# Optimization experiments

Hardware: AMD Instinct MI355X
Metric: run time of the kernel (lower is better)

The kernel has to match this reference:

```python
import jax, jax.numpy as jnp
import numpy as np
from jax import lax

DIM = 384
NH = 8
HD = DIM // NH
M = 16          # num_anchors
B = 16
HH = 64
WW = 64
N = HH * WW
STD = 0.02


def setup_inputs() -> dict:
    key = jax.random.key(0)
    ks = jax.random.split(key, 12)
    rn = lambda k, shape: (jax.random.normal(k, shape, jnp.float32) * STD)
    return {
        "x": jax.random.normal(ks[0], (B, N, DIM), jnp.float32),
        "H": HH,
        "W": WW,
        "saliency_w": rn(ks[1], (DIM, 1)),
        "saliency_b": jnp.zeros((1,), jnp.float32),
        "anchor_seeds": rn(ks[2], (1, M, DIM)),
        "w_q_agg": rn(ks[3], (DIM, DIM)),
        "w_kv_agg": rn(ks[4], (DIM, 2 * DIM)),
        "w_q_self": rn(ks[5], (DIM, DIM)),
        "w_kv_self": rn(ks[6], (DIM, 2 * DIM)),
        "w_q_bcast": rn(ks[7], (DIM, DIM)),
        "w_kv_bcast": rn(ks[8], (DIM, 2 * DIM)),
        "dw_kernel": rn(ks[9], (DIM, 1, 3, 3)),  # depthwise conv, OIHW with I=1
        "w_proj": rn(ks[10], (DIM, DIM)),
    }


def _mhsa(q_in, kv_in, wq, wkv):
    """Multi-head cross attention. q_in: [B,Lq,C], kv_in: [B,Lk,C]."""
    b, lq, c = q_in.shape
    lk = kv_in.shape[1]
    scale = HD ** -0.5
    q = (q_in @ wq).reshape(b, lq, NH, HD)
    kv = (kv_in @ wkv).reshape(b, lk, 2, NH, HD)
    k, v = kv[:, :, 0], kv[:, :, 1]
    attn = jnp.einsum("bqhd,bkhd->bhqk", q, k) * scale
    attn = jax.nn.softmax(attn, axis=-1)
    out = jnp.einsum("bhqk,bkhd->bqhd", attn, v).reshape(b, lq, c)
    return out


def reference(x, H, W, saliency_w, saliency_b, anchor_seeds,
              w_q_agg, w_kv_agg, w_q_self, w_kv_self,
              w_q_bcast, w_kv_bcast, dw_kernel, w_proj):
    b, n, c = x.shape
    # saliency gating
    sal = jax.nn.sigmoid(x @ saliency_w + saliency_b)  # [B,N,1]
    x_sal = x * sal
    # stage 1: anchors aggregate from saliency-gated tokens
    anchors = jnp.broadcast_to(anchor_seeds, (b, M, c))
    anchors = anchors + _mhsa(anchors, x_sal, w_q_agg, w_kv_agg)
    # stage 2: anchor self-attention
    anchors = anchors + _mhsa(anchors, anchors, w_q_self, w_kv_self)
    # stage 3: broadcast anchors back to all tokens
    global_out = _mhsa(x, anchors, w_q_bcast, w_kv_bcast)
    # depthwise 3x3 conv on the 2D token map
    x2d = x.reshape(b, H, W, c).transpose(0, 3, 1, 2)  # NCHW
    local = lax.conv_general_dilated(
        x2d, dw_kernel, window_strides=(1, 1), padding="SAME",
        feature_group_count=c,
        dimension_numbers=("NCHW", "OIHW", "NCHW"))
    local = local.transpose(0, 2, 3, 1).reshape(b, n, c)
    return (global_out + local) @ w_proj
```

## Files before the change

kernel.cpp:

```cpp
#include <hip/hip_runtime.h>
#include <hip/hip_bf16.h>

#define SCALE 0.14433756729740643f

typedef __attribute__((ext_vector_type(8))) short bf16x8;
typedef __attribute__((ext_vector_type(4))) float f32x4;

template <typename T> __device__ inline T cvt_from_f(float v);
template <> __device__ inline float cvt_from_f<float>(float v) { return v; }
template <> __device__ inline __hip_bfloat16 cvt_from_f<__hip_bfloat16>(float v) { return __float2bfloat16(v); }

__device__ inline void gload16(const void* g, void* l) {
  __builtin_amdgcn_global_load_lds((const __attribute__((address_space(1))) void*)g,
                                   (__attribute__((address_space(3))) void*)l, 16, 0, 0);
}

__device__ inline int xcd_flat(int nwg) {
  int flat = (blockIdx.z * gridDim.y + blockIdx.y) * gridDim.x + blockIdx.x;
  int per = nwg >> 3;
  return (flat & 7) * per + (flat >> 3);
}

__global__ __launch_bounds__(256) void prep(const float* __restrict__ x,
                                            const float* __restrict__ wsal,
                                            const float* __restrict__ bsal,
                                            __hip_bfloat16* __restrict__ xb,
                                            float* __restrict__ sal) {
  int wave = threadIdx.x >> 6, lane = threadIdx.x & 63;
  size_t row = (size_t)blockIdx.x * 4 + wave;
  const float* xr = x + row * 384;
  float xs[6];
  float part = 0.f;
#pragma unroll
  for (int j = 0; j < 6; j++) {
    int c = lane + 64 * j;
    xs[j] = xr[c];
    part += xs[j] * wsal[c];
  }
#pragma unroll
  for (int off = 32; off >= 1; off >>= 1) part += __shfl_xor(part, off);
  float s = 1.f / (1.f + __expf(-(part + bsal[0])));
#pragma unroll
  for (int j = 0; j < 6; j++) {
    int c = lane + 64 * j;
    xb[row * 384 + c] = __float2bfloat16(xs[j]);
  }
  if (lane == 0) sal[row] = s;
}

__global__ void wcast_tv(const float* __restrict__ w, __hip_bfloat16* __restrict__ wt) {
  int idx = blockIdx.x * 256 + threadIdx.x;
  if (idx >= 384 * 384) return;
  int n = idx / 384, k = idx % 384;
  wt[idx] = __float2bfloat16(w[(size_t)k * 768 + 384 + n]);
}

template <int K, typename OT, int BSHIFT>
__global__ __launch_bounds__(256) void gemm_mfma(const __hip_bfloat16* __restrict__ A,
                                                 const __hip_bfloat16* __restrict__ BT,
                                                 OT* __restrict__ out, int Ncols,
                                                 size_t btBatchStride) {
  __shared__ __align__(16) __hip_bfloat16 Asl[128][32];
  __shared__ __align__(16) __hip_bfloat16 Bsl[128][32];
  int nf = xcd_flat(gridDim.x * gridDim.y);
  int bX = nf % gridDim.x, bY = nf / gridDim.x;
  int tid = threadIdx.x;
  int lane = tid & 63;
  int w = tid >> 6;
  int wr = w >> 1, wc = w & 1;
  int fr = lane & 15, fq = lane >> 4;
  int rowBase = bY * 128, colBase = bX * 128;
  const __hip_bfloat16* BTb = BT + (size_t)(rowBase >> BSHIFT) * btBatchStride;

  int r1 = tid >> 2, kc1 = tid & 3;
  int r2 = (tid + 256) >> 2;

  char* aB1 = (char*)Asl + (size_t)(w * 64) * 16;
  char* aB2 = (char*)Asl + (size_t)(256 + w * 64) * 16;
  char* bB1 = (char*)Bsl + (size_t)(w * 64) * 16;
  char* bB2 = (char*)Bsl + (size_t)(256 + w * 64) * 16;

  const __hip_bfloat16* a1 = A + (size_t)(rowBase + r1) * K + kc1 * 8;
  const __hip_bfloat16* a2 = A + (size_t)(rowBase + r2) * K + kc1 * 8;
  const __hip_bfloat16* b1 = BTb + (size_t)(colBase + r1) * K + kc1 * 8;
  const __hip_bfloat16* b2 = BTb + (size_t)(colBase + r2) * K + kc1 * 8;

  f32x4 acc[4][4] = {};

  for (int kk = 0; kk < K; kk += 32) {
    gload16(a1 + kk, aB1);
    gload16(a2 + kk, aB2);
    gload16(b1 + kk, bB1);
    gload16(b2 + kk, bB2);
    __syncthreads();
    bf16x8 af[4], bfv[4];
#pragma unroll
    for (int m = 0; m < 4; m++) af[m] = *(const bf16x8*)&Asl[wr * 64 + m * 16 + fr][fq * 8];
#pragma unroll
    for (int n = 0; n < 4; n++) bfv[n] = *(const bf16x8*)&Bsl[wc * 64 + n * 16 + fr][fq * 8];
#pragma unroll
    for (int m = 0; m < 4; m++)
#pragma unroll
      for (int n = 0; n < 4; n++)
        acc[m][n] = __builtin_amdgcn_mfma_f32_16x16x32_bf16(af[m], bfv[n], acc[m][n], 0, 0, 0);
    __syncthreads();
  }

#pragma unroll
  for (int m = 0; m < 4; m++) {
    int row0 = rowBase + wr * 64 + m * 16 + fq * 4;
#pragma unroll
    for (int n = 0; n < 4; n++) {
      int col = colBase + wc * 64 + n * 16 + fr;
      f32x4 v = acc[m][n];
#pragma unroll
      for (int r = 0; r < 4; r++) out[(size_t)(row0 + r) * Ncols + col] = cvt_from_f<OT>(v[r]);
    }
  }
}

__global__ __launch_bounds__(256) void gemm_vlog(const __hip_bfloat16* __restrict__ A,
                                                 const __hip_bfloat16* __restrict__ BT,
                                                 __hip_bfloat16* __restrict__ vT,
                                                 __hip_bfloat16* __restrict__ lgT,
                                                 const float* __restrict__ rowScale) {
  constexpr int K = 384;
  __shared__ __align__(16) __hip_bfloat16 Asl[128][32];
  __shared__ __align__(16) __hip_bfloat16 Bsl[128][32];
  int nf = xcd_flat(2048);
  int bX = nf & 3, bY = nf >> 2;
  int tid = threadIdx.x;
  int lane = tid & 63;
  int w = tid >> 6;
  int wr = w >> 1, wc = w & 1;
  int fr = lane & 15, fq = lane >> 4;
  int rowBase = bY * 128, colBase = bX * 128;

  int r1 = tid >> 2, kc1 = tid & 3;
  int r2 = (tid + 256) >> 2;

  char* aB1 = (char*)Asl + (size_t)(w * 64) * 16;
  char* aB2 = (char*)Asl + (size_t)(256 + w * 64) * 16;
  char* bB1 = (char*)Bsl + (size_t)(w * 64) * 16;
  char* bB2 = (char*)Bsl + (size_t)(256 + w * 64) * 16;

  const __hip_bfloat16* a1 = A + (size_t)(rowBase + r1) * K + kc1 * 8;
  const __hip_bfloat16* a2 = A + (size_t)(rowBase + r2) * K + kc1 * 8;
  const __hip_bfloat16* b1 = BT + (size_t)(colBase + r1) * K + kc1 * 8;
  const __hip_bfloat16* b2 = BT + (size_t)(colBase + r2) * K + kc1 * 8;

  f32x4 acc[4][4] = {};

  for (int kk = 0; kk < K; kk += 32) {
    gload16(a1 + kk, aB1);
    gload16(a2 + kk, aB2);
    gload16(b1 + kk, bB1);
    gload16(b2 + kk, bB2);
    __syncthreads();
    bf16x8 af[4], bfv[4];
#pragma unroll
    for (int m = 0; m < 4; m++) af[m] = *(const bf16x8*)&Asl[wr * 64 + m * 16 + fr][fq * 8];
#pragma unroll
    for (int n = 0; n < 4; n++) bfv[n] = *(const bf16x8*)&Bsl[wc * 64 + n * 16 + fr][fq * 8];
#pragma unroll
    for (int m = 0; m < 4; m++)
#pragma unroll
      for (int n = 0; n < 4; n++)
        acc[m][n] = __builtin_amdgcn_mfma_f32_16x16x32_bf16(af[m], bfv[n], acc[m][n], 0, 0, 0);
    __syncthreads();
  }

  float sv[4][4];
#pragma unroll
  for (int m = 0; m < 4; m++)
#pragma unroll
    for (int r = 0; r < 4; r++)
      sv[m][r] = rowScale[rowBase + wr * 64 + m * 16 + fq * 4 + r];

  if (bX < 3) {
#pragma unroll
    for (int m = 0; m < 4; m++) {
      int row0 = rowBase + wr * 64 + m * 16 + fq * 4;
      int bb = row0 >> 12;
      int n0 = row0 & 4095;
#pragma unroll
      for (int n = 0; n < 4; n++) {
        int col = colBase + wc * 64 + n * 16 + fr;
        __hip_bfloat16 tb[4];
#pragma unroll
        for (int r = 0; r < 4; r++) tb[r] = __float2bfloat16(acc[m][n][r] * sv[m][r]);
        *(unsigned long long*)(vT + ((size_t)bb * 384 + col) * 4096 + n0) = *(unsigned long long*)tb;
      }
    }
  } else {
#pragma unroll
    for (int m = 0; m < 4; m++) {
      int row0 = rowBase + wr * 64 + m * 16 + fq * 4;
      int bb = row0 >> 12;
      int n0 = row0 & 4095;
#pragma unroll
      for (int n = 0; n < 4; n++) {
        int col = wc * 64 + n * 16 + fr;
        __hip_bfloat16 tb[4];
#pragma unroll
        for (int r = 0; r < 4; r++) tb[r] = __float2bfloat16(acc[m][n][r] * sv[m][r]);
        *(unsigned long long*)(lgT + ((size_t)bb * 128 + col) * 4096 + n0) = *(unsigned long long*)tb;
      }
    }
  }
}

__global__ __launch_bounds__(256) void gemm_pv(const __hip_bfloat16* __restrict__ PT,
                                               const __hip_bfloat16* __restrict__ vT,
                                               float* __restrict__ pbuf) {
  __shared__ __align__(16) __hip_bfloat16 Asl[128][32];
  __shared__ __align__(16) __hip_bfloat16 Bsl[128][32];
  int nf = xcd_flat(384);
  int bX = nf % 3, bY = (nf / 3) & 15, kz = nf / 48;
  int tid = threadIdx.x;
  int lane = tid & 63;
  int w = tid >> 6;
  int wr = w >> 1, wc = w & 1;
  int fr = lane & 15, fq = lane >> 4;
  int rowBase = bY * 128, colBase = bX * 128;
  const __hip_bfloat16* BTb = vT + (size_t)bY * 384 * 4096;

  int r1 = tid >> 2, kc1 = tid & 3;
  int r2 = (tid + 256) >> 2;

  char* aB1 = (char*)Asl + (size_t)(w * 64) * 16;
  char* aB2 = (char*)Asl + (size_t)(256 + w * 64) * 16;
  char* bB1 = (char*)Bsl + (size_t)(w * 64) * 16;
  char* bB2 = (char*)Bsl + (size_t)(256 + w * 64) * 16;

  const __hip_bfloat16* a1 = PT + (size_t)(rowBase + r1) * 4096 + kz * 512 + kc1 * 8;
  const __hip_bfloat16* a2 = PT + (size_t)(rowBase + r2) * 4096 + kz * 512 + kc1 * 8;
  const __hip_bfloat16* b1 = BTb + (size_t)(colBase + r1) * 4096 + kz * 512 + kc1 * 8;
  const __hip_bfloat16* b2 = BTb + (size_t)(colBase + r2) * 4096 + kz * 512 + kc1 * 8;

  f32x4 acc[4][4] = {};

  for (int kk = 0; kk < 512; kk += 32) {
    gload16(a1 + kk, aB1);
    gload16(a2 + kk, aB2);
    gload16(b1 + kk, bB1);
    gload16(b2 + kk, bB2);
    __syncthreads();
    bf16x8 af[4], bfv[4];
#pragma unroll
    for (int m = 0; m < 4; m++) af[m] = *(const bf16x8*)&Asl[wr * 64 + m * 16 + fr][fq * 8];
#pragma unroll
    for (int n = 0; n < 4; n++) bfv[n] = *(const bf16x8*)&Bsl[wc * 64 + n * 16 + fr][fq * 8];
#pragma unroll
    for (int m = 0; m < 4; m++)
#pragma unroll
      for (int n = 0; n < 4; n++)
        acc[m][n] = __builtin_amdgcn_mfma_f32_16x16x32_bf16(af[m], bfv[n], acc[m][n], 0, 0, 0);
    __syncthreads();
  }

  float* outz = pbuf + (size_t)kz * 786432;
#pragma unroll
  for (int m = 0; m < 4; m++) {
    int row0 = rowBase + wr * 64 + m * 16 + fq * 4;
#pragma unroll
    for (int n = 0; n < 4; n++) {
      int col = colBase + wc * 64 + n * 16 + fr;
      f32x4 v = acc[m][n];
#pragma unroll
      for (int r = 0; r < 4; r++) outz[(size_t)(row0 + r) * 384 + col] = v[r];
    }
  }
}

__global__ void anch_fix2(const float* __restrict__ pbuf, const float* __restrict__ seeds,
                          float* __restrict__ anch1) {
  int idx = blockIdx.x * 256 + threadIdx.x;
  int b = idx / 6144;
  int rem = idx - b * 6144;
  int m = rem / 384, c = rem - m * 384;
  int g = b * 128 + (c / 48) * 16 + m;
  const float* p = pbuf + (size_t)g * 384 + c;
  float s = 0.f;
#pragma unroll
  for (int z = 0; z < 8; z++) s += p[(size_t)z * 786432];
  anch1[idx] = seeds[rem] + s;
}

__global__ __launch_bounds__(256) void softmax_rows(const __hip_bfloat16* __restrict__ lgT,
                                                    __hip_bfloat16* __restrict__ PT) {
  int g = blockIdx.x;
  const __hip_bfloat16* row = lgT + (size_t)g * 4096;
  int tid = threadIdx.x, wv = tid >> 6, lane = tid & 63;
  __shared__ float redm[4], reds[4];
  float v[16];
  union { ulonglong2 u; __hip_bfloat16 h[8]; } L0, L1;
  L0.u = *(const ulonglong2*)(row + tid * 16);
  L1.u = *(const ulonglong2*)(row + tid * 16 + 8);
#pragma unroll
  for (int i = 0; i < 8; i++) {
    v[i] = __bfloat162float(L0.h[i]);
    v[8 + i] = __bfloat162float(L1.h[i]);
  }
  float mx = v[0];
#pragma unroll
  for (int i = 1; i < 16; i++) mx = fmaxf(mx, v[i]);
#pragma unroll
  for (int off = 1; off < 64; off <<= 1) mx = fmaxf(mx, __shfl_xor(mx, off));
  if (lane == 0) redm[wv] = mx;
  __syncthreads();
  mx = fmaxf(fmaxf(redm[0], redm[1]), fmaxf(redm[2], redm[3]));
  float s = 0.f;
#pragma unroll
  for (int i = 0; i < 16; i++) {
    v[i] = __expf(v[i] - mx);
    s += v[i];
  }
#pragma unroll
  for (int off = 1; off < 64; off <<= 1) s += __shfl_xor(s, off);
  if (lane == 0) reds[wv] = s;
  __syncthreads();
  s = (reds[0] + reds[1]) + (reds[2] + reds[3]);
  float inv = 1.f / s;
  __hip_bfloat16 tb[16];
#pragma unroll
  for (int i = 0; i < 16; i++) tb[i] = __float2bfloat16(v[i] * inv);
  __hip_bfloat16* op = PT + (size_t)g * 4096 + tid * 16;
  *(ulonglong2*)op = *(ulonglong2*)tb;
  *(ulonglong2*)(op + 8) = *(ulonglong2*)(tb + 8);
}

__global__ void fill_wl(const float* __restrict__ wkv, const float* __restrict__ qseed,
                        __hip_bfloat16* __restrict__ wvlT) {
  int idx = blockIdx.x * 256 + threadIdx.x;
  int hm = idx / 384, ci = idx - hm * 384;
  int h = hm >> 4, m = hm & 15;
  const float* wp = wkv + (size_t)ci * 768 + h * 48;
  const float* qp = qseed + m * 384 + h * 48;
  float acc = 0.f;
#pragma unroll
  for (int d = 0; d < 48; d++) acc += wp[d] * qp[d];
  wvlT[384 * 384 + idx] = __float2bfloat16(acc);
}

__global__ __launch_bounds__(256) void wtrans(const float* __restrict__ wproj,
                                              __hip_bfloat16* __restrict__ bt2) {
  __shared__ float t[64][65];
  int kt = blockIdx.x * 64, ct = blockIdx.y * 64;
  int tid = threadIdx.x;
  int c = tid & 63, r4 = tid >> 6;
#pragma unroll
  for (int i = 0; i < 16; i++) {
    int r = i * 4 + r4;
    t[r][c] = wproj[(size_t)(kt + r) * 384 + ct + c];
  }
  __syncthreads();
  __hip_bfloat16 vals[16];
#pragma unroll
  for (int i = 0; i < 16; i++) vals[i] = __float2bfloat16(t[c][i * 4 + r4]);
  for (int b = blockIdx.z * 4; b < blockIdx.z * 4 + 4; b++) {
    __hip_bfloat16* dst = bt2 + (size_t)b * 196608;
#pragma unroll
    for (int i = 0; i < 16; i++) {
      int rr = i * 4 + r4;
      dst[(size_t)(ct + rr) * 512 + kt + c] = vals[i];
    }
  }
}

__global__ __launch_bounds__(256) void fill_fold(const float* __restrict__ wq,
                                                 const float* __restrict__ wproj,
                                                 const float* __restrict__ kvb,
                                                 __hip_bfloat16* __restrict__ wpbT,
                                                 __hip_bfloat16* __restrict__ bt2) {
  int b = blockIdx.y;
  int tid = threadIdx.x;
  __shared__ float stage[16][48];
  __shared__ __hip_bfloat16 obuf[16][264];
  if (blockIdx.x < 8) {
    int h = blockIdx.x;
    for (int idx = tid; idx < 768; idx += 256) {
      int m = idx / 48, d = idx % 48;
      stage[m][d] = kvb[(size_t)(b * 16 + m) * 768 + h * 48 + d];
    }
    __syncthreads();
    for (int kbase = 0; kbase < 384; kbase += 256) {
      int chunk = (kbase == 0) ? 256 : 128;
      if (tid < chunk) {
        int k = kbase + tid;
        const float4* wp = (const float4*)(wq + (size_t)k * 384 + h * 48);
        float acc[16] = {};
#pragma unroll
        for (int dq = 0; dq < 12; dq++) {
          float4 wv = wp[dq];
#pragma unroll
          for (int m = 0; m < 16; m++)
            acc[m] += stage[m][dq * 4] * wv.x + stage[m][dq * 4 + 1] * wv.y +
                      stage[m][dq * 4 + 2] * wv.z + stage[m][dq * 4 + 3] * wv.w;
        }
#pragma unroll
        for (int m = 0; m < 16; m++) obuf[m][tid] = __float2bfloat16(acc[m]);
      }
      __syncthreads();
      for (int widx = tid; widx < 16 * chunk; widx += 256) {
        int m = widx / chunk, kk = widx - m * chunk;
        wpbT[(size_t)b * 49152 + (size_t)(h * 16 + m) * 384 + kbase + kk] = obuf[m][kk];
      }
      __syncthreads();
    }
  } else {
    int h = blockIdx.x - 8;
    for (int idx = tid; idx < 768; idx += 256) {
      int m = idx / 48, d = idx % 48;
      stage[m][d] = kvb[(size_t)(b * 16 + m) * 768 + 384 + h * 48 + d];
    }
    __syncthreads();
    for (int cp = tid; cp < 384; cp += 256) {
      float acc[16] = {};
      for (int d = 0; d < 48; d++) {
        float wv = wproj[(size_t)(h * 48 + d) * 384 + cp];
#pragma unroll
        for (int m = 0; m < 16; m++) acc[m] += stage[m][d] * wv;
      }
      __hip_bfloat16 tb[16];
#pragma unroll
      for (int m = 0; m < 16; m++) tb[m] = __float2bfloat16(acc[m]);
      __hip_bfloat16* dst = bt2 + (size_t)b * 196608 + (size_t)cp * 512 + 384 + h * 16;
      *(ulonglong2*)dst = *(ulonglong2*)tb;
      *(ulonglong2*)(dst + 8) = *(ulonglong2*)(tb + 8);
    }
  }
}

__global__ __launch_bounds__(256) void pgemm(const __hip_bfloat16* __restrict__ A,
                                             const __hip_bfloat16* __restrict__ wpbT,
                                             __hip_bfloat16* __restrict__ A2) {
  constexpr int K = 384;
  __shared__ __align__(16) __hip_bfloat16 Asl[128][32];
  __shared__ __align__(16) __hip_bfloat16 Bsl[128][32];
  int tid = threadIdx.x;
  int lane = tid & 63;
  int w = tid >> 6;
  int wr = w >> 1, wc = w & 1;
  int fr = lane & 15, fq = lane >> 4;
  int rowBase = blockIdx.y * 128;
  const __hip_bfloat16* BTb = wpbT + (size_t)(rowBase >> 12) * (128 * 384);

  int r1 = tid >> 2, kc1 = tid & 3;
  int r2 = (tid + 256) >> 2;

  char* aB1 = (char*)Asl + (size_t)(w * 64) * 16;
  char* aB2 = (char*)Asl + (size_t)(256 + w * 64) * 16;
  char* bB1 = (char*)Bsl + (size_t)(w * 64) * 16;
  char* bB2 = (char*)Bsl + (size_t)(256 + w * 64) * 16;

  const __hip_bfloat16* a1 = A + (size_t)(rowBase + r1) * K + kc1 * 8;
  const __hip_bfloat16* a2 = A + (size_t)(rowBase + r2) * K + kc1 * 8;
  const __hip_bfloat16* b1 = BTb + (size_t)r1 * K + kc1 * 8;
  const __hip_bfloat16* b2 = BTb + (size_t)r2 * K + kc1 * 8;

  f32x4 acc[4][4] = {};

  for (int kk = 0; kk < K; kk += 32) {
    gload16(a1 + kk, aB1);
    gload16(a2 + kk, aB2);
    gload16(b1 + kk, bB1);
    gload16(b2 + kk, bB2);
    __syncthreads();
    bf16x8 af[4], bfv[4];
#pragma unroll
    for (int m = 0; m < 4; m++) af[m] = *(const bf16x8*)&Asl[wr * 64 + m * 16 + fr][fq * 8];
#pragma unroll
    for (int n = 0; n < 4; n++) bfv[n] = *(const bf16x8*)&Bsl[wc * 64 + n * 16 + fr][fq * 8];
#pragma unroll
    for (int m = 0; m < 4; m++)
#pragma unroll
      for (int n = 0; n < 4; n++)
        acc[m][n] = __builtin_amdgcn_mfma_f32_16x16x32_bf16(af[m], bfv[n], acc[m][n], 0, 0, 0);
    __syncthreads();
  }

#pragma unroll
  for (int m = 0; m < 4; m++) {
    int row0 = rowBase + wr * 64 + m * 16 + fq * 4;
#pragma unroll
    for (int n = 0; n < 4; n++) {
      int col = wc * 64 + n * 16 + fr;
      f32x4 v = acc[m][n];
      f32x4 mx = v;
#pragma unroll
      for (int off = 1; off < 16; off <<= 1)
#pragma unroll
        for (int r = 0; r < 4; r++) mx[r] = fmaxf(mx[r], __shfl_xor(mx[r], off));
      f32x4 e;
#pragma unroll
      for (int r = 0; r < 4; r++) e[r] = __expf(v[r] - mx[r]);
      f32x4 s = e;
#pragma unroll
      for (int off = 1; off < 16; off <<= 1)
#pragma unroll
        for (int r = 0; r < 4; r++) s[r] += __shfl_xor(s[r], off);
#pragma unroll
      for (int r = 0; r < 4; r++)
        A2[(size_t)(row0 + r) * 512 + 384 + col] = __float2bfloat16(e[r] / s[r]);
    }
  }
}

__global__ __launch_bounds__(256) void dwconv3(const __hip_bfloat16* __restrict__ xb,
                                               const float* __restrict__ dwk,
                                               __hip_bfloat16* __restrict__ A2) {
  int b = blockIdx.y;
  int y = blockIdx.x;
  int w = threadIdx.x >> 6, lane = threadIdx.x & 63;
  int c0 = lane * 6;
  int x0 = w * 16;
  float kw[9][6];
#pragma unroll
  for (int ki = 0; ki < 9; ki++)
#pragma unroll
    for (int i = 0; i < 6; i++) kw[ki][i] = dwk[(c0 + i) * 9 + ki];

  const __hip_bfloat16* base = xb + ((size_t)(b * 4096 + y * 64)) * 384 + c0;
  bool yv[3];
#pragma unroll
  for (int t = 0; t < 3; t++) {
    int yy = y + t - 1;
    yv[t] = (yy >= 0 && yy < 64);
  }

  float colL[3][6], colC[3][6], colR[3][6];
  auto loadcol = [&](float (&dst)[3][6], int x) {
#pragma unroll
    for (int t = 0; t < 3; t++) {
      if (yv[t]) {
        const __hip_bfloat16* p = base + ((size_t)(t - 1) * 64 + x) * 384;
#pragma unroll
        for (int i = 0; i < 6; i++) dst[t][i] = __bfloat162float(p[i]);
      } else {
#pragma unroll
        for (int i = 0; i < 6; i++) dst[t][i] = 0.f;
      }
    }
  };

  if (x0 == 0) {
#pragma unroll
    for (int t = 0; t < 3; t++)
#pragma unroll
      for (int i = 0; i < 6; i++) colL[t][i] = 0.f;
  } else {
    loadcol(colL, x0 - 1);
  }
  loadcol(colC, x0);

  for (int step = 0; step < 16; step++) {
    int x = x0 + step;
    if (x + 1 < 64) {
      loadcol(colR, x + 1);
    } else {
#pragma unroll
      for (int t = 0; t < 3; t++)
#pragma unroll
        for (int i = 0; i < 6; i++) colR[t][i] = 0.f;
    }
    float acc[6];
#pragma unroll
    for (int i = 0; i < 6; i++) {
      float a = 0.f;
#pragma unroll
      for (int t = 0; t < 3; t++)
        a += colL[t][i] * kw[t * 3 + 0][i] + colC[t][i] * kw[t * 3 + 1][i] +
             colR[t][i] * kw[t * 3 + 2][i];
      acc[i] = a;
    }
    __hip_bfloat16 tb[6];
#pragma unroll
    for (int i = 0; i < 6; i++) tb[i] = __float2bfloat16(acc[i]);
    __hip_bfloat16* gp = A2 + ((size_t)(b * 4096 + y * 64 + x)) * 512 + c0;
    *(unsigned int*)(gp) = *(unsigned int*)(tb);
    *(unsigned int*)(gp + 2) = *(unsigned int*)(tb + 2);
    *(unsigned int*)(gp + 4) = *(unsigned int*)(tb + 4);
#pragma unroll
    for (int t = 0; t < 3; t++)
#pragma unroll
      for (int i = 0; i < 6; i++) {
        colL[t][i] = colC[t][i];
        colC[t][i] = colR[t][i];
      }
  }
}

__global__ __launch_bounds__(256) void anchor_proj2(const float* __restrict__ A,
                                                    const float* __restrict__ W,
                                                    float* __restrict__ out, int wstride,
                                                    int scaleCols) {
  int cs = blockIdx.x * 16;
  int b = blockIdx.y;
  __shared__ float a1[16][385];
  int tid = threadIdx.x;
  for (int idx = tid; idx < 6144; idx += 256) a1[idx / 384][idx % 384] = A[b * 6144 + idx];
  __syncthreads();
  int m = tid >> 4, cc = tid & 15;
  int col = cs + cc;
  const float* wp = W + col;
  float acc0 = 0.f, acc1 = 0.f, acc2 = 0.f, acc3 = 0.f;
#pragma unroll 4
  for (int k = 0; k < 384; k += 4) {
    acc0 += a1[m][k] * wp[(size_t)k * wstride];
    acc1 += a1[m][k + 1] * wp[(size_t)(k + 1) * wstride];
    acc2 += a1[m][k + 2] * wp[(size_t)(k + 2) * wstride];
    acc3 += a1[m][k + 3] * wp[(size_t)(k + 3) * wstride];
  }
  float acc = (acc0 + acc1) + (acc2 + acc3);
  if (col < scaleCols) acc *= SCALE;
  out[((size_t)b * 16 + m) * wstride + col] = acc;
}

__global__ __launch_bounds__(256) void anchor_proj_qkv(const float* __restrict__ A,
                                                       const float* __restrict__ Wq,
                                                       const float* __restrict__ Wkv,
                                                       float* __restrict__ q_out,
                                                       float* __restrict__ kv_out) {
  bool isQ = blockIdx.x < 24;
  int bx = isQ ? blockIdx.x : blockIdx.x - 24;
  const float* W = isQ ? Wq : Wkv;
  float* outp = isQ ? q_out : kv_out;
  int wstride = isQ ? 384 : 768;
  float scale = isQ ? SCALE : 1.f;
  int cs = bx * 16;
  int b = blockIdx.y;
  __shared__ float a1[16][385];
  int tid = threadIdx.x;
  for (int idx = tid; idx < 6144; idx += 256) a1[idx / 384][idx % 384] = A[b * 6144 + idx];
  __syncthreads();
  int m = tid >> 4, cc = tid & 15;
  int col = cs + cc;
  const float* wp = W + col;
  float acc0 = 0.f, acc1 = 0.f, acc2 = 0.f, acc3 = 0.f;
#pragma unroll 4
  for (int k = 0; k < 384; k += 4) {
    acc0 += a1[m][k] * wp[(size_t)k * wstride];
    acc1 += a1[m][k + 1] * wp[(size_t)(k + 1) * wstride];
    acc2 += a1[m][k + 2] * wp[(size_t)(k + 2) * wstride];
    acc3 += a1[m][k + 3] * wp[(size_t)(k + 3) * wstride];
  }
  float acc = ((acc0 + acc1) + (acc2 + acc3)) * scale;
  outp[((size_t)b * 16 + m) * wstride + col] = acc;
}

__global__ void self_attn(const float* __restrict__ qsf, const float* __restrict__ kvs,
                          const float* __restrict__ anch1, float* __restrict__ anch2) {
  int h = blockIdx.x & 7, b = blockIdx.x >> 3;
  __shared__ float qs[16][48], ks[16][48], vs[16][48], p[16][17];
  int tid = threadIdx.x;
  for (int idx = tid; idx < 768; idx += 256) {
    int m = idx / 48, d = idx % 48;
    qs[m][d] = qsf[(b * 16 + m) * 384 + h * 48 + d];
    ks[m][d] = kvs[(b * 16 + m) * 768 + h * 48 + d];
    vs[m][d] = kvs[(b * 16 + m) * 768 + 384 + h * 48 + d];
  }
  __syncthreads();
  {
    int mq = tid >> 4, mk = tid & 15;
    float acc = 0.f;
    for (int d = 0; d < 48; d++) acc += qs[mq][d] * ks[mk][d];
    p[mq][mk] = acc;
  }
  __syncthreads();
  if (tid < 16) {
    float mx = -1e30f;
    for (int mk = 0; mk < 16; mk++) mx = fmaxf(mx, p[tid][mk]);
    float sum = 0.f;
    for (int mk = 0; mk < 16; mk++) {
      float e = __expf(p[tid][mk] - mx);
      p[tid][mk] = e;
      sum += e;
    }
    float inv = 1.f / sum;
    for (int mk = 0; mk < 16; mk++) p[tid][mk] *= inv;
  }
  __syncthreads();
  for (int idx = tid; idx < 768; idx += 256) {
    int m = idx / 48, d = idx % 48;
    float acc = 0.f;
    for (int mk = 0; mk < 16; mk++) acc += p[m][mk] * vs[mk][d];
    int c = h * 48 + d;
    anch2[(b * 16 + m) * 384 + c] = anch1[(b * 16 + m) * 384 + c] + acc;
  }
}

extern "C" void kernel_launch(void* const* d_in, const int* in_sizes, int n_in,
                              void* d_out, int out_size, void* d_ws, size_t ws_size,
                              hipStream_t stream) {
  (void)in_sizes; (void)n_in; (void)out_size; (void)ws_size;
  const float* x = (const float*)d_in[0];
  const float* wsal = (const float*)d_in[3];
  const float* bsal = (const float*)d_in[4];
  const float* seeds = (const float*)d_in[5];
  const float* w_q_agg = (const float*)d_in[6];
  const float* w_kv_agg = (const float*)d_in[7];
  const float* w_q_self = (const float*)d_in[8];
  const float* w_kv_self = (const float*)d_in[9];
  const float* w_q_bcast = (const float*)d_in[10];
  const float* w_kv_bcast = (const float*)d_in[11];
  const float* dwk = (const float*)d_in[12];
  const float* w_proj = (const float*)d_in[13];
  float* out = (float*)d_out;

  char* ws = (char*)d_ws;
  size_t off = 0;
  auto take = [&](size_t bytes) -> void* {
    void* p = ws + off;
    off += (bytes + 255) & ~(size_t)255;
    return p;
  };
  __hip_bfloat16* xb = (__hip_bfloat16*)take(50331648);
  __hip_bfloat16* vT = (__hip_bfloat16*)take(50331648);
  char* lgRegion = (char*)take(33554432);
  __hip_bfloat16* PT = (__hip_bfloat16*)take(16777216);
  float* qseed = (float*)take(24576);
  float* sal = (float*)take(262144);
  float* anch1 = (float*)take(393216);
  float* anch2 = (float*)take(393216);
  float* q_self = (float*)take(393216);
  float* kv_self = (float*)take(786432);
  float* kv_b = (float*)take(786432);
  __hip_bfloat16* wvlT = (__hip_bfloat16*)take(393216);
  __hip_bfloat16* wpbT = (__hip_bfloat16*)take(1572864);
  __hip_bfloat16* bt2 = (__hip_bfloat16*)take(6291456);
  __hip_bfloat16* logitsT = (__hip_bfloat16*)lgRegion;
  float* pbuf = (float*)lgRegion;
  __hip_bfloat16* A2 = vT;

  prep<<<16384, 256, 0, stream>>>(x, wsal, bsal, xb, sal);
  anchor_proj2<<<dim3(24, 1), 256, 0, stream>>>(seeds, w_q_agg, qseed, 384, 384);
  wcast_tv<<<576, 256, 0, stream>>>(w_kv_agg, wvlT);
  fill_wl<<<192, 256, 0, stream>>>(w_kv_agg, qseed, wvlT);
  wtrans<<<dim3(6, 6, 4), 256, 0, stream>>>(w_proj, bt2);
  gemm_vlog<<<dim3(4, 512), 256, 0, stream>>>(xb, wvlT, vT, logitsT, sal);
  softmax_rows<<<2048, 256, 0, stream>>>(logitsT, PT);
  gemm_pv<<<dim3(3, 16, 8), 256, 0, stream>>>(PT, vT, pbuf);
  anch_fix2<<<384, 256, 0, stream>>>(pbuf, seeds, anch1);
  anchor_proj_qkv<<<dim3(72, 16), 256, 0, stream>>>(anch1, w_q_self, w_kv_self, q_self, kv_self);
  self_attn<<<128, 256, 0, stream>>>(q_self, kv_self, anch1, anch2);
  anchor_proj2<<<dim3(48, 16), 256, 0, stream>>>(anch2, w_kv_bcast, kv_b, 768, 384);
  fill_fold<<<dim3(16, 16), 256, 0, stream>>>(w_q_bcast, w_proj, kv_b, wpbT, bt2);
  pgemm<<<dim3(1, 512), 256, 0, stream>>>(xb, wpbT, A2);
  dwconv3<<<dim3(64, 16), 256, 0, stream>>>(xb, dwk, A2);
  gemm_mfma<512, float, 12><<<dim3(3, 512), 256, 0, stream>>>(A2, bt2, out, 384, (size_t)384 * 512);
}
```

Measured before the change: 345.3 us.

## Reassociate stage-1 attention to apply P to x before the value projection

```diff
diff --git a/kernel.cpp b/kernel.cpp
--- a/kernel.cpp
+++ b/kernel.cpp
@@ -119,22 +119,19 @@
   }
 }
 
-__global__ __launch_bounds__(256) void gemm_vlog(const __hip_bfloat16* __restrict__ A,
-                                                 const __hip_bfloat16* __restrict__ BT,
-                                                 __hip_bfloat16* __restrict__ vT,
-                                                 __hip_bfloat16* __restrict__ lgT,
-                                                 const float* __restrict__ rowScale) {
+__global__ __launch_bounds__(256) void gemm_logits(const __hip_bfloat16* __restrict__ A,
+                                                   const __hip_bfloat16* __restrict__ BT,
+                                                   __hip_bfloat16* __restrict__ lgT,
+                                                   const float* __restrict__ rowScale) {
   constexpr int K = 384;
   __shared__ __align__(16) __hip_bfloat16 Asl[128][32];
   __shared__ __align__(16) __hip_bfloat16 Bsl[128][32];
-  int nf = xcd_flat(2048);
-  int bX = nf & 3, bY = nf >> 2;
   int tid = threadIdx.x;
   int lane = tid & 63;
   int w = tid >> 6;
   int wr = w >> 1, wc = w & 1;
   int fr = lane & 15, fq = lane >> 4;
-  int rowBase = bY * 128, colBase = bX * 128;
+  int rowBase = blockIdx.x * 128;
 
   int r1 = tid >> 2, kc1 = tid & 3;
   int r2 = (tid + 256) >> 2;
@@ -146,8 +143,8 @@
 
   const __hip_bfloat16* a1 = A + (size_t)(rowBase + r1) * K + kc1 * 8;
   const __hip_bfloat16* a2 = A + (size_t)(rowBase + r2) * K + kc1 * 8;
-  const __hip_bfloat16* b1 = BT + (size_t)(colBase + r1) * K + kc1 * 8;
-  const __hip_bfloat16* b2 = BT + (size_t)(colBase + r2) * K + kc1 * 8;
+  const __hip_bfloat16* b1 = BT + (size_t)r1 * K + kc1 * 8;
+  const __hip_bfloat16* b2 = BT + (size_t)r2 * K + kc1 * 8;
 
   f32x4 acc[4][4] = {};
 
@@ -177,117 +174,24 @@
     for (int r = 0; r < 4; r++)
       sv[m][r] = rowScale[rowBase + wr * 64 + m * 16 + fq * 4 + r];
 
-  if (bX < 3) {
-#pragma unroll
-    for (int m = 0; m < 4; m++) {
-      int row0 = rowBase + wr * 64 + m * 16 + fq * 4;
-      int bb = row0 >> 12;
-      int n0 = row0 & 4095;
-#pragma unroll
-      for (int n = 0; n < 4; n++) {
-        int col = colBase + wc * 64 + n * 16 + fr;
-        __hip_bfloat16 tb[4];
-#pragma unroll
-        for (int r = 0; r < 4; r++) tb[r] = __float2bfloat16(acc[m][n][r] * sv[m][r]);
-        *(unsigned long long*)(vT + ((size_t)bb * 384 + col) * 4096 + n0) = *(unsigned long long*)tb;
-      }
-    }
-  } else {
-#pragma unroll
-    for (int m = 0; m < 4; m++) {
-      int row0 = rowBase + wr * 64 + m * 16 + fq * 4;
-      int bb = row0 >> 12;
-      int n0 = row0 & 4095;
-#pragma unroll
-      for (int n = 0; n < 4; n++) {
-        int col = wc * 64 + n * 16 + fr;
-        __hip_bfloat16 tb[4];
-#pragma unroll
-        for (int r = 0; r < 4; r++) tb[r] = __float2bfloat16(acc[m][n][r] * sv[m][r]);
-        *(unsigned long long*)(lgT + ((size_t)bb * 128 + col) * 4096 + n0) = *(unsigned long long*)tb;
-      }
-    }
-  }
-}
-
-__global__ __launch_bounds__(256) void gemm_pv(const __hip_bfloat16* __restrict__ PT,
-                                               const __hip_bfloat16* __restrict__ vT,
-                                               float* __restrict__ pbuf) {
-  __shared__ __align__(16) __hip_bfloat16 Asl[128][32];
-  __shared__ __align__(16) __hip_bfloat16 Bsl[128][32];
-  int nf = xcd_flat(384);
-  int bX = nf % 3, bY = (nf / 3) & 15, kz = nf / 48;
-  int tid = threadIdx.x;
-  int lane = tid & 63;
-  int w = tid >> 6;
-  int wr = w >> 1, wc = w & 1;
-  int fr = lane & 15, fq = lane >> 4;
-  int rowBase = bY * 128, colBase = bX * 128;
-  const __hip_bfloat16* BTb = vT + (size_t)bY * 384 * 4096;
-
-  int r1 = tid >> 2, kc1 = tid & 3;
-  int r2 = (tid + 256) >> 2;
-
-  char* aB1 = (char*)Asl + (size_t)(w * 64) * 16;
-  char* aB2 = (char*)Asl + (size_t)(256 + w * 64) * 16;
-  char* bB1 = (char*)Bsl + (size_t)(w * 64) * 16;
-  char* bB2 = (char*)Bsl + (size_t)(256 + w * 64) * 16;
-
-  const __hip_bfloat16* a1 = PT + (size_t)(rowBase + r1) * 4096 + kz * 512 + kc1 * 8;
-  const __hip_bfloat16* a2 = PT + (size_t)(rowBase + r2) * 4096 + kz * 512 + kc1 * 8;
-  const __hip_bfloat16* b1 = BTb + (size_t)(colBase + r1) * 4096 + kz * 512 + kc1 * 8;
-  const __hip_bfloat16* b2 = BTb + (size_t)(colBase + r2) * 4096 + kz * 512 + kc1 * 8;
-
-  f32x4 acc[4][4] = {};
-
-  for (int kk = 0; kk < 512; kk += 32) {
-    gload16(a1 + kk, aB1);
-    gload16(a2 + kk, aB2);
-    gload16(b1 + kk, bB1);
-    gload16(b2 + kk, bB2);
-    __syncthreads();
-    bf16x8 af[4], bfv[4];
-#pragma unroll
-    for (int m = 0; m < 4; m++) af[m] = *(const bf16x8*)&Asl[wr * 64 + m * 16 + fr][fq * 8];
-#pragma unroll
-    for (int n = 0; n < 4; n++) bfv[n] = *(const bf16x8*)&Bsl[wc * 64 + n * 16 + fr][fq * 8];
-#pragma unroll
-    for (int m = 0; m < 4; m++)
-#pragma unroll
-      for (int n = 0; n < 4; n++)
-        acc[m][n] = __builtin_amdgcn_mfma_f32_16x16x32_bf16(af[m], bfv[n], acc[m][n], 0, 0, 0);
-    __syncthreads();
-  }
-
-  float* outz = pbuf + (size_t)kz * 786432;
 #pragma unroll
   for (int m = 0; m < 4; m++) {
     int row0 = rowBase + wr * 64 + m * 16 + fq * 4;
+    int bb = row0 >> 12;
+    int n0 = row0 & 4095;
 #pragma unroll
     for (int n = 0; n < 4; n++) {
-      int col = colBase + wc * 64 + n * 16 + fr;
-      f32x4 v = acc[m][n];
-#pragma unroll
-      for (int r = 0; r < 4; r++) outz[(size_t)(row0 + r) * 384 + col] = v[r];
-    }
-  }
-}
-
-__global__ void anch_fix2(const float* __restrict__ pbuf, const float* __restrict__ seeds,
-                          float* __restrict__ anch1) {
-  int idx = blockIdx.x * 256 + threadIdx.x;
-  int b = idx / 6144;
-  int rem = idx - b * 6144;
-  int m = rem / 384, c = rem - m * 384;
-  int g = b * 128 + (c / 48) * 16 + m;
-  const float* p = pbuf + (size_t)g * 384 + c;
-  float s = 0.f;
-#pragma unroll
-  for (int z = 0; z < 8; z++) s += p[(size_t)z * 786432];
-  anch1[idx] = seeds[rem] + s;
+      int col = wc * 64 + n * 16 + fr;
+      __hip_bfloat16 tb[4];
+#pragma unroll
+      for (int r = 0; r < 4; r++) tb[r] = __float2bfloat16(acc[m][n][r] * sv[m][r]);
+      *(unsigned long long*)(lgT + ((size_t)bb * 128 + col) * 4096 + n0) = *(unsigned long long*)tb;
+    }
+  }
 }
 
 __global__ __launch_bounds__(256) void softmax_rows(const __hip_bfloat16* __restrict__ lgT,
+                                                    const float* __restrict__ sal,
                                                     __hip_bfloat16* __restrict__ PT) {
   int g = blockIdx.x;
   const __hip_bfloat16* row = lgT + (size_t)g * 4096;
@@ -322,12 +226,109 @@
   __syncthreads();
   s = (reds[0] + reds[1]) + (reds[2] + reds[3]);
   float inv = 1.f / s;
+  const float* sp = sal + (size_t)(g >> 7) * 4096 + tid * 16;
+  float salv[16];
+#pragma unroll
+  for (int i = 0; i < 4; i++) {
+    float4 q = *(const float4*)(sp + i * 4);
+    salv[i * 4] = q.x; salv[i * 4 + 1] = q.y; salv[i * 4 + 2] = q.z; salv[i * 4 + 3] = q.w;
+  }
   __hip_bfloat16 tb[16];
 #pragma unroll
-  for (int i = 0; i < 16; i++) tb[i] = __float2bfloat16(v[i] * inv);
+  for (int i = 0; i < 16; i++) tb[i] = __float2bfloat16(v[i] * inv * salv[i]);
   __hip_bfloat16* op = PT + (size_t)g * 4096 + tid * 16;
   *(ulonglong2*)op = *(ulonglong2*)tb;
   *(ulonglong2*)(op + 8) = *(ulonglong2*)(tb + 8);
+}
+
+__global__ __launch_bounds__(256) void gemm_pvx(const __hip_bfloat16* __restrict__ PT,
+                                                const __hip_bfloat16* __restrict__ xb,
+                                                float* __restrict__ pbuf) {
+  __shared__ __align__(16) __hip_bfloat16 Asl[128][32];
+  __shared__ __align__(16) short Bsl[128][40];
+  int nf = xcd_flat(384);
+  int bX = nf % 3, bY = (nf / 3) & 15, kz = nf / 48;
+  int tid = threadIdx.x;
+  int lane = tid & 63;
+  int w = tid >> 6;
+  int wr = w >> 1, wc = w & 1;
+  int fr = lane & 15, fq = lane >> 4;
+  int rowBase = bY * 128, colBase = bX * 128;
+
+  int r1 = tid >> 2, kc1 = tid & 3;
+  int r2 = (tid + 256) >> 2;
+  char* aB1 = (char*)Asl + (size_t)(w * 64) * 16;
+  char* aB2 = (char*)Asl + (size_t)(256 + w * 64) * 16;
+  const __hip_bfloat16* a1 = PT + (size_t)(rowBase + r1) * 4096 + kz * 512 + kc1 * 8;
+  const __hip_bfloat16* a2 = PT + (size_t)(rowBase + r2) * 4096 + kz * 512 + kc1 * 8;
+
+  int nl1 = tid >> 4;
+  int cc = tid & 15;
+  const __hip_bfloat16* Bg0 = xb + ((size_t)bY * 4096 + kz * 512) * 384 + colBase + cc * 8;
+
+  f32x4 acc[4][4] = {};
+
+  for (int kk = 0; kk < 512; kk += 32) {
+    gload16(a1 + kk, aB1);
+    gload16(a2 + kk, aB2);
+    const __hip_bfloat16* Bg = Bg0 + (size_t)kk * 384;
+    bf16x8 rb1 = *(const bf16x8*)(Bg + (size_t)nl1 * 384);
+    bf16x8 rb2 = *(const bf16x8*)(Bg + (size_t)(nl1 + 16) * 384);
+#pragma unroll
+    for (int j = 0; j < 8; j++) {
+      Bsl[cc * 8 + j][nl1] = rb1[j];
+      Bsl[cc * 8 + j][nl1 + 16] = rb2[j];
+    }
+    __syncthreads();
+    bf16x8 af[4], bfv[4];
+#pragma unroll
+    for (int m = 0; m < 4; m++) af[m] = *(const bf16x8*)&Asl[wr * 64 + m * 16 + fr][fq * 8];
+#pragma unroll
+    for (int n = 0; n < 4; n++) bfv[n] = *(const bf16x8*)&Bsl[wc * 64 + n * 16 + fr][fq * 8];
+#pragma unroll
+    for (int m = 0; m < 4; m++)
+#pragma unroll
+      for (int n = 0; n < 4; n++)
+        acc[m][n] = __builtin_amdgcn_mfma_f32_16x16x32_bf16(af[m], bfv[n], acc[m][n], 0, 0, 0);
+    __syncthreads();
+  }
+
+  float* outz = pbuf + (size_t)kz * 786432;
+#pragma unroll
+  for (int m = 0; m < 4; m++) {
+    int row0 = rowBase + wr * 64 + m * 16 + fq * 4;
+#pragma unroll
+    for (int n = 0; n < 4; n++) {
+      int col = colBase + wc * 64 + n * 16 + fr;
+      f32x4 v = acc[m][n];
+#pragma unroll
+      for (int r = 0; r < 4; r++) outz[(size_t)(row0 + r) * 384 + col] = v[r];
+    }
+  }
+}
+
+__global__ __launch_bounds__(256) void reduce_z(const float* __restrict__ pbuf,
+                                                __hip_bfloat16* __restrict__ pvx) {
+  int i4 = (blockIdx.x * 256 + threadIdx.x) * 4;
+  float4 s = *(const float4*)(pbuf + i4);
+#pragma unroll
+  for (int z = 1; z < 8; z++) {
+    float4 t = *(const float4*)(pbuf + (size_t)z * 786432 + i4);
+    s.x += t.x; s.y += t.y; s.z += t.z; s.w += t.w;
+  }
+  __hip_bfloat16 tb[4] = {__float2bfloat16(s.x), __float2bfloat16(s.y),
+                          __float2bfloat16(s.z), __float2bfloat16(s.w)};
+  *(unsigned long long*)(pvx + i4) = *(unsigned long long*)tb;
+}
+
+__global__ void anch_fix(const float* __restrict__ outF, const float* __restrict__ seeds,
+                         float* __restrict__ anch1) {
+  int idx = blockIdx.x * 256 + threadIdx.x;
+  int b = idx / 6144;
+  int rem = idx - b * 6144;
+  int m = rem / 384, c = rem - m * 384;
+  int h = c / 48;
+  anch1[idx] = seeds[rem] + outF[((size_t)b * 128 + h * 16 + m) * 384 + c];
 }
 
 __global__ void fill_wl(const float* __restrict__ wkv, const float* __restrict__ qseed,
@@ -716,9 +717,10 @@
     return p;
   };
   __hip_bfloat16* xb = (__hip_bfloat16*)take(50331648);
-  __hip_bfloat16* vT = (__hip_bfloat16*)take(50331648);
-  char* lgRegion = (char*)take(33554432);
+  char* R = (char*)take(67108864);
   __hip_bfloat16* PT = (__hip_bfloat16*)take(16777216);
+  __hip_bfloat16* pvx = (__hip_bfloat16*)take(1572864);
+  float* outF = (float*)take(3145728);
   float* qseed = (float*)take(24576);
   float* sal = (float*)take(262144);
   float* anch1 = (float*)take(393216);
@@ -729,19 +731,21 @@
   __hip_bfloat16* wvlT = (__hip_bfloat16*)take(393216);
   __hip_bfloat16* wpbT = (__hip_bfloat16*)take(1572864);
   __hip_bfloat16* bt2 = (__hip_bfloat16*)take(6291456);
-  __hip_bfloat16* logitsT = (__hip_bfloat16*)lgRegion;
-  float* pbuf = (float*)lgRegion;
-  __hip_bfloat16* A2 = vT;
+  __hip_bfloat16* logitsT = (__hip_bfloat16*)R;
+  float* pbuf = (float*)R;
+  __hip_bfloat16* A2 = (__hip_bfloat16*)R;
 
   prep<<<16384, 256, 0, stream>>>(x, wsal, bsal, xb, sal);
   anchor_proj2<<<dim3(24, 1), 256, 0, stream>>>(seeds, w_q_agg, qseed, 384, 384);
   wcast_tv<<<576, 256, 0, stream>>>(w_kv_agg, wvlT);
   fill_wl<<<192, 256, 0, stream>>>(w_kv_agg, qseed, wvlT);
   wtrans<<<dim3(6, 6, 4), 256, 0, stream>>>(w_proj, bt2);
-  gemm_vlog<<<dim3(4, 512), 256, 0, stream>>>(xb, wvlT, vT, logitsT, sal);
-  softmax_rows<<<2048, 256, 0, stream>>>(logitsT, PT);
-  gemm_pv<<<dim3(3, 16, 8), 256, 0, stream>>>(PT, vT, pbuf);
-  anch_fix2<<<384, 256, 0, stream>>>(pbuf, seeds, anch1);
+  gemm_logits<<<512, 256, 0, stream>>>(xb, wvlT + 384 * 384, logitsT, sal);
+  softmax_rows<<<2048, 256, 0, stream>>>(logitsT, sal, PT);
+  gemm_pvx<<<dim3(3, 16, 8), 256, 0, stream>>>(PT, xb, pbuf);
+  reduce_z<<<768, 256, 0, stream>>>(pbuf, pvx);
+  gemm_mfma<384, float, 12><<<dim3(3, 16), 256, 0, stream>>>(pvx, wvlT, outF, 384, 0);
+  anch_fix<<<384, 256, 0, stream>>>(outF, seeds, anch1);
   anchor_proj_qkv<<<dim3(72, 16), 256, 0, stream>>>(anch1, w_q_self, w_kv_self, q_self, kv_self);
   self_attn<<<128, 256, 0, stream>>>(q_self, kv_self, anch1, anch2);
   anchor_proj2<<<dim3(48, 16), 256, 0, stream>>>(anch2, w_kv_bcast, kv_b, 768, 384);
```

Measured after the change: 350.6 us. No clear change (+1.5%).
